# Kernel tuning notes

Hardware: AMD Instinct MI355X
Metric: run time of the kernel (lower is better)

The kernel has to match this reference:

```python
import jax, jax.numpy as jnp
import numpy as np

EMBED = 1024
HEADS = 16
HEAD_SIZE = 64


def setup_inputs() -> dict:
    key = jax.random.key(0)
    ks = jax.random.split(key, 6)
    B, T = 2, 2048
    s = EMBED ** -0.5
    x = jax.random.normal(ks[0], (B, T, EMBED), dtype=jnp.float32)
    Wk = jax.random.normal(ks[1], (EMBED, HEADS * HEAD_SIZE), dtype=jnp.float32) * s
    Wq = jax.random.normal(ks[2], (EMBED, HEADS * HEAD_SIZE), dtype=jnp.float32) * s
    Wv = jax.random.normal(ks[3], (EMBED, HEADS * HEAD_SIZE), dtype=jnp.float32) * s
    Wp = jax.random.normal(ks[4], (HEADS * HEAD_SIZE, EMBED), dtype=jnp.float32) * s
    bp = jax.random.normal(ks[5], (EMBED,), dtype=jnp.float32) * 0.01
    return {"x": x, "Wk": Wk, "Wq": Wq, "Wv": Wv, "Wp": Wp, "bp": bp}


def reference(x, Wk, Wq, Wv, Wp, bp):
    # x: [B, T, C]; dropout in eval mode (identity), matching inference semantics
    B, T, C = x.shape
    def split_heads(y):  # [B,T,H*Dh] -> [B,H,T,Dh]
        return y.reshape(B, T, HEADS, HEAD_SIZE).transpose(0, 2, 1, 3)
    q = split_heads(x @ Wq)
    k = split_heads(x @ Wk)
    v = split_heads(x @ Wv)
    scale = HEAD_SIZE ** -0.5
    wei = jnp.einsum('bhqd,bhkd->bhqk', q, k) * scale  # [B,H,T,T]
    causal = jnp.tril(jnp.ones((T, T), dtype=bool))
    wei = jnp.where(causal, wei, -jnp.inf)
    wei = jax.nn.softmax(wei, axis=-1)
    out = jnp.einsum('bhqk,bhkd->bhqd', wei, v)  # [B,H,T,Dh]
    out = out.transpose(0, 2, 1, 3).reshape(B, T, HEADS * HEAD_SIZE)
    return out @ Wp + bp
```

## Files before the change

kernel.cpp:

```cpp
#include <hip/hip_runtime.h>
#include <stdint.h>


typedef unsigned short bfu;
typedef unsigned int u32;
typedef short bf16x8 __attribute__((ext_vector_type(8)));
typedef float f32x4 __attribute__((ext_vector_type(4)));
typedef float f32x16 __attribute__((ext_vector_type(16)));

#define DEVI static __device__ __forceinline__

DEVI bfu f2bf(float f) {
  union { float f; unsigned u; } a; a.f = f;
  unsigned u = a.u;
  u += 0x7fffu + ((u >> 16) & 1u);
  return (bfu)(u >> 16);
}

DEVI float bf2f(bfu x) {
  union { u32 u; float f; } a; a.u = ((u32)x) << 16; return a.f;
}

DEVI void gld_lds16(const void* g, void* l) {
  __builtin_amdgcn_global_load_lds(
      (const __attribute__((address_space(1))) void*)g,
      (__attribute__((address_space(3))) void*)l, 16, 0, 0);
}

#define BAR_VM4()                                         \
  do {                                                    \
    asm volatile("s_waitcnt vmcnt(4)" ::: "memory");      \
    __builtin_amdgcn_s_barrier();                         \
    asm volatile("" ::: "memory");                        \
  } while (0)
#define BAR_VM0()                                         \
  do {                                                    \
    asm volatile("s_waitcnt vmcnt(0)" ::: "memory");      \
    __builtin_amdgcn_s_barrier();                         \
    asm volatile("" ::: "memory");                        \
  } while (0)


__global__ __launch_bounds__(256) void conv_x(const float* __restrict__ x,
                                              bfu* __restrict__ xb) {
  const int n4 = (4096 * 1024) / 4;
  for (int i = blockIdx.x * 256 + threadIdx.x; i < n4; i += gridDim.x * 256) {
    float4 v = ((const float4*)x)[i];
    ushort4 p;
    p.x = f2bf(v.x); p.y = f2bf(v.y); p.z = f2bf(v.z); p.w = f2bf(v.w);
    ((ushort4*)xb)[i] = p;
  }
}

__global__ __launch_bounds__(256) void conv_w(
    const float* __restrict__ W0, const float* __restrict__ W1,
    const float* __restrict__ W2, const float* __restrict__ W3,
    bfu* __restrict__ T0, bfu* __restrict__ T1,
    bfu* __restrict__ T2, bfu* __restrict__ T3) {
  __shared__ bfu tile[64][65];
  const float* W; bfu* T;
  switch (blockIdx.z) {
    case 0:  W = W0; T = T0; break;
    case 1:  W = W1; T = T1; break;
    case 2:  W = W2; T = T2; break;
    default: W = W3; T = T3; break;
  }
  const int k0 = blockIdx.y * 64, n0 = blockIdx.x * 64;
  const int c = threadIdx.x & 63, r4 = threadIdx.x >> 6;
#pragma unroll
  for (int i = 0; i < 16; i++) {
    int row = r4 + i * 4;
    tile[row][c] = f2bf(W[(size_t)(k0 + row) * 1024 + n0 + c]);
  }
  __syncthreads();
#pragma unroll
  for (int i = 0; i < 16; i++) {
    int row = r4 + i * 4;
    T[(size_t)(n0 + row) * 1024 + k0 + c] = tile[c][row];
  }
}


DEVI void gemm128_core(const bfu* __restrict__ A, const bfu* __restrict__ Bt,
                       int K, int m0, int n0, bfu* As, bfu* Bs, int tid,
                       f32x4 acc[4][4]) {
  const int lane = tid & 63, wave = tid >> 6;
  const int wr = wave >> 1, wc = wave & 1;
  const int fr = lane & 15, fq = lane >> 4;
  const int r_a = tid >> 2;
  const int koff = ((tid & 3) ^ ((tid >> 3) & 3)) * 8;
  const int rslot = (fq ^ ((fr >> 1) & 3)) * 8;
#define GSTAGE(buf, k0s)                                                              \
  do {                                                                                \
    gld_lds16(A  + (size_t)(m0 +      r_a) * K + (k0s) + koff,                        \
              As + (buf) * 4096 + tid * 8);                                           \
    gld_lds16(A  + (size_t)(m0 + 64 + r_a) * K + (k0s) + koff,                        \
              As + (buf) * 4096 + 2048 + tid * 8);                                    \
    gld_lds16(Bt + (size_t)(n0 +      r_a) * K + (k0s) + koff,                        \
              Bs + (buf) * 4096 + tid * 8);                                           \
    gld_lds16(Bt + (size_t)(n0 + 64 + r_a) * K + (k0s) + koff,                        \
              Bs + (buf) * 4096 + 2048 + tid * 8);                                    \
  } while (0)
  const int NS = K >> 5;
  GSTAGE(0, 0);
  GSTAGE(1, 32);
  BAR_VM4();
  for (int i = 0; i < NS; i++) {
    if (i + 2 < NS) GSTAGE((i + 2) % 3, (i + 2) * 32);
    const bfu* AsC = As + (i % 3) * 4096;
    const bfu* BsC = Bs + (i % 3) * 4096;
    bf16x8 af[4], bfv[4];
#pragma unroll
    for (int m = 0; m < 4; m++)
      af[m] = *(const bf16x8*)&AsC[(wr * 64 + m * 16 + fr) * 32 + rslot];
#pragma unroll
    for (int n = 0; n < 4; n++)
      bfv[n] = *(const bf16x8*)&BsC[(wc * 64 + n * 16 + fr) * 32 + rslot];
#pragma unroll
    for (int m = 0; m < 4; m++)
#pragma unroll
      for (int n = 0; n < 4; n++)
        acc[m][n] = __builtin_amdgcn_mfma_f32_16x16x32_bf16(af[m], bfv[n],
                                                            acc[m][n], 0, 0, 0);
    if (i + 2 < NS) BAR_VM4();
    else            BAR_VM0();
  }
#undef GSTAGE
}

__global__ __launch_bounds__(256) void gemm_qkv(
    const bfu* __restrict__ A, const bfu* __restrict__ Wqt,
    const bfu* __restrict__ Wkt, const bfu* __restrict__ Wvt,
    bfu* __restrict__ Qb, bfu* __restrict__ Kb, bfu* __restrict__ Vb) {
  __shared__ __align__(16) bfu As[3 * 4096];
  __shared__ __align__(16) bfu Bs[3 * 4096];
  const int bid = blockIdx.x;
  const int xcd = bid & 7, i0 = bid >> 3;
  const int tz = i0 >> 5, rem = i0 & 31;
  const int tx = rem >> 2, ty = xcd * 4 + (rem & 3);
  const bfu* Bt; bfu* out; int epi;
  if (tz == 0)      { Bt = Wqt; out = Qb; epi = 0; }
  else if (tz == 1) { Bt = Wkt; out = Kb; epi = 0; }
  else              { Bt = Wvt; out = Vb; epi = 1; }
  const float qs = (tz == 0) ? 0.1803368801f : 1.0f;
  const int m0 = ty * 128, n0 = tx * 128;
  const int tid = threadIdx.x, lane = tid & 63, wave = tid >> 6;
  const int wr = wave >> 1, wc = wave & 1, fr = lane & 15, fq = lane >> 4;
  f32x4 acc[4][4] = {};
  gemm128_core(A, Bt, 1024, m0, n0, As, Bs, tid, acc);
#pragma unroll
  for (int m = 0; m < 4; m++)
#pragma unroll
    for (int n = 0; n < 4; n++) {
      int r = m0 + wr * 64 + m * 16 + fq * 4;
      int c = n0 + wc * 64 + n * 16 + fr;
      int b = r >> 11, t = r & 2047, h = c >> 6, d = c & 63;
      if (epi == 0) {
        size_t base = ((size_t)(b * 16 + h) * 2048 + t) * 64 + d;
#pragma unroll
        for (int i = 0; i < 4; i++)
          out[base + (size_t)i * 64] = f2bf(acc[m][n][i] * qs);
      } else {
        size_t base = ((size_t)(b * 16 + h) * 64 + d) * 2048 + t;
        ushort4 p;
        p.x = f2bf(acc[m][n][0]); p.y = f2bf(acc[m][n][1]);
        p.z = f2bf(acc[m][n][2]); p.w = f2bf(acc[m][n][3]);
        *(ushort4*)&out[base] = p;
      }
    }
}

__global__ __launch_bounds__(256) void gemm_proj(
    const bfu* __restrict__ A, const bfu* __restrict__ Bt,
    const float* __restrict__ bias, float* __restrict__ out) {
  __shared__ __align__(16) bfu As[3 * 4096];
  __shared__ __align__(16) bfu Bs[3 * 4096];
  const int bid = blockIdx.x;
  const int xcd = bid & 7, i0 = bid >> 3;
  const int tx = i0 >> 2, ty = xcd * 4 + (i0 & 3);
  const int m0 = ty * 128, n0 = tx * 128;
  const int tid = threadIdx.x, lane = tid & 63, wave = tid >> 6;
  const int wr = wave >> 1, wc = wave & 1, fr = lane & 15, fq = lane >> 4;
  f32x4 acc[4][4] = {};
  gemm128_core(A, Bt, 1024, m0, n0, As, Bs, tid, acc);
#pragma unroll
  for (int m = 0; m < 4; m++)
#pragma unroll
    for (int n = 0; n < 4; n++) {
      int r = m0 + wr * 64 + m * 16 + fq * 4;
      int c = n0 + wc * 64 + n * 16 + fr;
      float bv = bias[c];
#pragma unroll
      for (int i = 0; i < 4; i++)
        out[(size_t)(r + i) * 1024 + c] = acc[m][n][i] + bv;
    }
}


__global__ __launch_bounds__(256) void attn_fwd(
    const bfu* __restrict__ Q, const bfu* __restrict__ K,
    const bfu* __restrict__ Vt, bfu* __restrict__ Ob,
    bfu* __restrict__ PO, float* __restrict__ PM, float* __restrict__ PL) {
  __shared__ __align__(16) bfu Ks[2][64 * 64];
  __shared__ __align__(16) bfu Vs[2][64 * 64];
  const int bid = blockIdx.x;
  const int xcd = bid & 7, i0 = bid >> 3;
  const int slot = i0 >> 5, cuL = i0 & 31;
  const int head = cuL >> 3, cu8 = cuL & 7;
  const int hb = xcd * 4 + head;
  int qb, mode;
  if (slot < 2)      { qb = 15 - cu8; mode = slot + 1; }
  else if (cu8 < 4)  { if (slot == 3) return; qb = cu8; mode = 0; }
  else               { qb = cu8; mode = slot - 1; }
  const int kb0   = (mode == 2) ? (qb + 1) : 0;
  const int kbmax = (mode == 1) ? qb : (2 * qb + 1);
  const int tid = threadIdx.x, wave = tid >> 6, lane = tid & 63;
  const int q31 = lane & 31, hi = lane >> 5;
  const bfu* Qh = Q  + (size_t)hb * 2048 * 64;
  const bfu* Kh = K  + (size_t)hb * 2048 * 64;
  const bfu* Vh = Vt + (size_t)hb * 64 * 2048;
  const int b = hb >> 4, h = hb & 15;
  const int q0w = qb * 128 + wave * 32;
  const int qg = q0w + q31;

  const int r0 = tid >> 3, r1 = (256 + tid) >> 3;
  const int c0 = (tid & 7) ^ (r0 & 7), c1 = (tid & 7) ^ (r1 & 7);
#define STAGE(bufi, kbase)                                                            \
  do {                                                                                \
    gld_lds16(Kh + (size_t)((kbase) + r0) * 64 + c0 * 8, &Ks[bufi][tid * 8]);         \
    gld_lds16(Kh + (size_t)((kbase) + r1) * 64 + c1 * 8, &Ks[bufi][(256 + tid) * 8]); \
    gld_lds16(Vh + (size_t)r0 * 2048 + (kbase) + c0 * 8, &Vs[bufi][tid * 8]);         \
    gld_lds16(Vh + (size_t)r1 * 2048 + (kbase) + c1 * 8, &Vs[bufi][(256 + tid) * 8]); \
  } while (0)

  bf16x8 qv[4];
#pragma unroll
  for (int c = 0; c < 4; c++)
    qv[c] = *(const bf16x8*)&Qh[(size_t)(q0w + q31) * 64 + c * 16 + hi * 8];

  bf16x8 onesv;
#pragma unroll
  for (int j = 0; j < 8; j++) onesv[j] = (short)0x3F80;

  f32x16 o0 = {}, o1 = {}, lac = {};
  float m = -1e30f;

  STAGE(0, kb0 * 64);
  __syncthreads();

  int cc = 0;
  for (int kb = kb0; kb <= kbmax; kb++, cc ^= 1) {
    const int cur = cc;
    if (kb < kbmax) STAGE(cur ^ 1, (kb + 1) * 64);
    const int kbase = kb * 64;
    if (kbase <= q0w + 31) {
      const bfu* KsC = Ks[cur];
      const bfu* VsC = Vs[cur];
      f32x16 s0 = {}, s1 = {};
#pragma unroll
      for (int c = 0; c < 4; c++) {
        const int g = 2 * c + hi;
        bf16x8 kf0 = *(const bf16x8*)&KsC[(q31 * 8 + (g ^ (q31 & 7))) * 8];
        bf16x8 kf1 = *(const bf16x8*)&KsC[((32 + q31) * 8 + (g ^ (q31 & 7))) * 8];
        s0 = __builtin_amdgcn_mfma_f32_32x32x16_bf16(kf0, qv[c], s0, 0, 0, 0);
        s1 = __builtin_amdgcn_mfma_f32_32x32x16_bf16(kf1, qv[c], s1, 0, 0, 0);
      }
      if (kbase + 63 > q0w) {
#pragma unroll
        for (int r = 0; r < 16; r++) {
          int krow = (r & 3) + 8 * (r >> 2) + 4 * hi;
          if (kbase + krow > qg)      s0[r] = -1e30f;
          if (kbase + 32 + krow > qg) s1[r] = -1e30f;
        }
      }
      float pm = s0[0];
#pragma unroll
      for (int r = 1; r < 16; r++) pm = fmaxf(pm, s0[r]);
#pragma unroll
      for (int r = 0; r < 16; r++) pm = fmaxf(pm, s1[r]);
      pm = fmaxf(pm, __shfl_xor(pm, 32));
      if (!__all(pm <= m + 8.0f)) {
        float mn = fmaxf(m, pm);
        float al = __builtin_amdgcn_exp2f(m - mn);
        m = mn;
#pragma unroll
        for (int r = 0; r < 16; r++) {
          float alq = __shfl(al, (r & 3) + 8 * (r >> 2) + 4 * hi);
          o0[r] *= alq; o1[r] *= alq; lac[r] *= alq;
        }
      }
      u32 W0[8], W1[8];
#pragma unroll
      for (int w = 0; w < 8; w++) {
        float a0 = __builtin_amdgcn_exp2f(s0[2 * w] - m);
        float a1 = __builtin_amdgcn_exp2f(s0[2 * w + 1] - m);
        asm("v_cvt_pk_bf16_f32 %0, %1, %2" : "=v"(W0[w]) : "v"(a0), "v"(a1));
        float b0 = __builtin_amdgcn_exp2f(s1[2 * w] - m);
        float b1 = __builtin_amdgcn_exp2f(s1[2 * w + 1] - m);
        asm("v_cvt_pk_bf16_f32 %0, %1, %2" : "=v"(W1[w]) : "v"(b0), "v"(b1));
      }
      __builtin_amdgcn_s_setprio(1);
#pragma unroll
      for (int c = 0; c < 4; c++) {
        const u32* Wsel = (c < 2) ? W0 : W1;
        const int w0 = 4 * (c & 1);
        u32 t0 = Wsel[w0],     t2 = Wsel[w0 + 2];
        u32 t1 = Wsel[w0 + 1], t3 = Wsel[w0 + 3];
        asm("v_permlane32_swap_b32 %0, %1" : "+v"(t0), "+v"(t2));
        asm("v_permlane32_swap_b32 %0, %1" : "+v"(t1), "+v"(t3));
        union { u32 u[4]; bf16x8 v; } pa;
        pa.u[0] = t0; pa.u[1] = t1; pa.u[2] = t2; pa.u[3] = t3;
        const int g = 2 * c + hi;
        bf16x8 vb0 = *(const bf16x8*)&VsC[(q31 * 8 + (g ^ (q31 & 7))) * 8];
        bf16x8 vb1 = *(const bf16x8*)&VsC[((32 + q31) * 8 + (g ^ (q31 & 7))) * 8];
        o0  = __builtin_amdgcn_mfma_f32_32x32x16_bf16(pa.v, vb0,   o0,  0, 0, 0);
        o1  = __builtin_amdgcn_mfma_f32_32x32x16_bf16(pa.v, vb1,   o1,  0, 0, 0);
        lac = __builtin_amdgcn_mfma_f32_32x32x16_bf16(pa.v, onesv, lac, 0, 0, 0);
      }
      __builtin_amdgcn_s_setprio(0);
    }
    __syncthreads();
  }
#undef STAGE

  if (mode == 0) {
#pragma unroll
    for (int r = 0; r < 16; r++) {
      int t = q0w + (r & 3) + 8 * (r >> 2) + 4 * hi;
      float inv = 1.0f / lac[r];
      size_t base = (size_t)(b * 2048 + t) * 1024 + h * 64;
      Ob[base + q31]      = f2bf(o0[r] * inv);
      Ob[base + 32 + q31] = f2bf(o1[r] * inv);
    }
  } else {
    const int p = (hb * 12 + (qb - 4)) * 2 + (mode - 1);
    bfu*   po = PO + (size_t)p * 8192;
    float* pmv = PM + p * 128;
    float* plv = PL + p * 128;
    pmv[wave * 32 + q31] = m;
#pragma unroll
    for (int r = 0; r < 16; r++) {
      int rm = (r & 3) + 8 * (r >> 2) + 4 * hi;
      plv[wave * 32 + rm] = lac[r];
      po[(wave * 32 + rm) * 64 + q31]      = f2bf(o0[r]);
      po[(wave * 32 + rm) * 64 + 32 + q31] = f2bf(o1[r]);
    }
  }
}

__global__ __launch_bounds__(256) void attn_comb(
    const bfu* __restrict__ PO, const float* __restrict__ PM,
    const float* __restrict__ PL, bfu* __restrict__ Ob) {
  const int g = blockIdx.x;
  const int hb = g / 12, j = g % 12, qb = j + 4;
  const int b = hb >> 4, h = hb & 15;
  const int p0 = g * 2, p1 = p0 + 1;
  const int tid = threadIdx.x;
  const int r = tid >> 1, ch = tid & 1;
  float m0 = PM[p0 * 128 + r], m1 = PM[p1 * 128 + r];
  float l0 = PL[p0 * 128 + r], l1 = PL[p1 * 128 + r];
  float ms = fmaxf(m0, m1);
  float f0 = __builtin_amdgcn_exp2f(m0 - ms);
  float f1 = __builtin_amdgcn_exp2f(m1 - ms);
  float inv = 1.0f / (l0 * f0 + l1 * f1);
  const bfu* a0 = PO + (size_t)p0 * 8192 + r * 64 + ch * 32;
  const bfu* a1 = PO + (size_t)p1 * 8192 + r * 64 + ch * 32;
  const int t = qb * 128 + r;
  bfu* ob = Ob + (size_t)(b * 2048 + t) * 1024 + h * 64 + ch * 32;
#pragma unroll
  for (int k = 0; k < 4; k++) {
    bf16x8 v0 = *(const bf16x8*)(a0 + k * 8);
    bf16x8 v1 = *(const bf16x8*)(a1 + k * 8);
    bf16x8 vo;
#pragma unroll
    for (int e = 0; e < 8; e++) {
      float acc = bf2f((bfu)(unsigned short)v0[e]) * f0 +
                  bf2f((bfu)(unsigned short)v1[e]) * f1;
      vo[e] = (short)f2bf(acc * inv);
    }
    *(bf16x8*)(ob + k * 8) = vo;
  }
}


extern "C" void kernel_launch(void* const* d_in, const int* in_sizes, int n_in,
                              void* d_out, int out_size, void* d_ws, size_t ws_size,
                              hipStream_t stream) {
  const float* x  = (const float*)d_in[0];
  const float* Wk = (const float*)d_in[1];
  const float* Wq = (const float*)d_in[2];
  const float* Wv = (const float*)d_in[3];
  const float* Wp = (const float*)d_in[4];
  const float* bp = (const float*)d_in[5];
  char* ws = (char*)d_ws;
  bfu* xb  = (bfu*)(ws);
  bfu* Wqt = (bfu*)(ws + ( 8u << 20));
  bfu* Wkt = (bfu*)(ws + (10u << 20));
  bfu* Wvt = (bfu*)(ws + (12u << 20));
  bfu* Wpt = (bfu*)(ws + (14u << 20));
  bfu* Qb  = (bfu*)(ws + (16u << 20));
  bfu* Kb  = (bfu*)(ws + (24u << 20));
  bfu* Vb  = (bfu*)(ws + (32u << 20));
  bfu* Ab  = (bfu*)(ws + (40u << 20));
  bfu*   PO = (bfu*)(ws);
  float* PM = (float*)(ws + (13u << 20));
  float* PL = (float*)(ws + (13u << 20) + (512u << 10));
  float* out = (float*)d_out;

  conv_x<<<1024, 256, 0, stream>>>(x, xb);
  conv_w<<<dim3(16, 16, 4), 256, 0, stream>>>(Wq, Wk, Wv, Wp, Wqt, Wkt, Wvt, Wpt);
  gemm_qkv<<<768, 256, 0, stream>>>(xb, Wqt, Wkt, Wvt, Qb, Kb, Vb);
  attn_fwd<<<1024, 256, 0, stream>>>(Qb, Kb, Vb, Ab, PO, PM, PL);
  attn_comb<<<384, 256, 0, stream>>>(PO, PM, PL, Ab);
  gemm_proj<<<256, 256, 0, stream>>>(Ab, Wpt, bp, out);
}
```

Before: 136.1 us.

## Replace QKV GEMM with a fused 256x256-tile double-buffered 512-thread kernel

Replaces the 128x128-tile QKV projection with one kernel that treats the contiguous transposed Wq/Wk/Wv as a single 3072-wide B matrix. It computes 256x256 output tiles with 8 waves and double-buffered LDS staging. Global-to-LDS loads for the next K tile are interleaved with MFMA quarters, and s_setprio raises priority during the MFMA bursts. The aim is more operand reuse per load and better overlap of loads with compute. The risk is that only 192 workgroups are launched, fewer than the CU count, which leaves some CUs idle, and the larger accumulator footprint puts pressure on registers.

```diff
diff --git a/kernel.cpp b/kernel.cpp
--- a/kernel.cpp
+++ b/kernel.cpp
@@ -78,6 +78,120 @@
     int row = r4 + i * 4;
     T[(size_t)(n0 + row) * 1024 + k0 + c] = tile[c][row];
   }
+}
+
+
+__global__ __launch_bounds__(512) void gemm_qkv256(
+    const bfu* __restrict__ A, const bfu* __restrict__ Bt,
+    bfu* __restrict__ Qb, bfu* __restrict__ Kb, bfu* __restrict__ Vb) {
+  __shared__ __align__(16) bfu LDS[2 * 32768];
+  const int bid = blockIdx.x;
+  const int xcd = bid & 7, i0 = bid >> 3;
+  const int tx = i0 >> 1, ty = xcd * 2 + (i0 & 1);
+  const int z = tx >> 2;
+  const int m0 = ty * 256, n0g = tx * 256;
+  const int tid = threadIdx.x, wave = tid >> 6, lane = tid & 63;
+  const int wr = wave >> 2, wc = wave & 3;
+  const int fr = lane & 15, fq = lane >> 4;
+  const int rslot4 = fq ^ ((fr >> 1) & 3);
+
+#define STAGE_HT(bufn, ktile, isB, kk)                                           \
+  do {                                                                           \
+    const bfu* srcb = (isB) ? Bt + (size_t)n0g * 1024 : A + (size_t)m0 * 1024;   \
+    bfu* dstb = LDS + (bufn) * 32768 + ((isB) ? 16384 : 0) + (kk) * 8192;        \
+    _Pragma("unroll")                                                            \
+    for (int j_ = 0; j_ < 2; j_++) {                                             \
+      int s_ = tid + j_ * 512;                                                   \
+      int r_ = s_ >> 2, cg_ = (s_ & 3) ^ ((r_ >> 1) & 3);                        \
+      gld_lds16(srcb + (size_t)r_ * 1024 + (ktile) * 64 + (kk) * 32 + cg_ * 8,   \
+                dstb + s_ * 8);                                                  \
+    }                                                                            \
+  } while (0)
+
+#define READ_B(kk)                                                               \
+  _Pragma("unroll")                                                              \
+  for (int n = 0; n < 4; n++)                                                    \
+    bfv[n] = *(const bf16x8*)&bufc_p[16384 + (kk) * 8192 +                       \
+              ((wc * 64 + n * 16 + fr) * 4 + rslot4) * 8];
+
+#define READ_A(dst, mq, kk)                                                      \
+  _Pragma("unroll")                                                              \
+  for (int mm = 0; mm < 4; mm++)                                                 \
+    dst[mm] = *(const bf16x8*)&bufc_p[(kk) * 8192 +                              \
+              ((wr * 128 + ((mq) * 4 + mm) * 16 + fr) * 4 + rslot4) * 8];
+
+#define MFMA_Q(afv, mq)                                                          \
+  __builtin_amdgcn_s_setprio(1);                                                 \
+  _Pragma("unroll")                                                              \
+  for (int mm = 0; mm < 4; mm++)                                                 \
+    _Pragma("unroll")                                                            \
+    for (int n = 0; n < 4; n++)                                                  \
+      acc[(mq) * 4 + mm][n] = __builtin_amdgcn_mfma_f32_16x16x32_bf16(           \
+          afv[mm], bfv[n], acc[(mq) * 4 + mm][n], 0, 0, 0);                      \
+  __builtin_amdgcn_s_setprio(0);
+
+  f32x4 acc[8][4] = {};
+  STAGE_HT(0, 0, 0, 0);
+  STAGE_HT(0, 0, 1, 0);
+  STAGE_HT(0, 0, 0, 1);
+  STAGE_HT(0, 0, 1, 1);
+  BAR_VM4();
+
+  const int NT = 16;
+  for (int t = 0; t < NT; t++) {
+    const int more = (t + 1 < NT);
+    const bfu* bufc_p = LDS + (t & 1) * 32768;
+    const int bufn = (t & 1) ^ 1;
+    bf16x8 bfv[4], afA[4], afB[4];
+    READ_B(0);
+    READ_A(afA, 0, 0);
+    if (more) STAGE_HT(bufn, t + 1, 0, 0);
+    MFMA_Q(afA, 0);
+    READ_A(afB, 1, 0);
+    if (more) STAGE_HT(bufn, t + 1, 1, 0);
+    MFMA_Q(afB, 1);
+    if (more) BAR_VM4();
+    else      BAR_VM0();
+    READ_B(1);
+    READ_A(afA, 0, 1);
+    if (more) STAGE_HT(bufn, t + 1, 0, 1);
+    MFMA_Q(afA, 0);
+    READ_A(afB, 1, 1);
+    if (more) STAGE_HT(bufn, t + 1, 1, 1);
+    MFMA_Q(afB, 1);
+    BAR_VM4();
+  }
+#undef STAGE_HT
+#undef READ_B
+#undef READ_A
+#undef MFMA_Q
+
+  const float qs = (z == 0) ? 0.1803368801f : 1.0f;
+#pragma unroll
+  for (int mf = 0; mf < 8; mf++)
+#pragma unroll
+    for (int n = 0; n < 4; n++) {
+      int r = m0 + wr * 128 + mf * 16 + fq * 4;
+      int cwm = (tx & 3) * 256 + wc * 64 + n * 16 + fr;
+      int b = r >> 11, tt = r & 2047, h = cwm >> 6, d = cwm & 63;
+      if (z == 0) {
+        size_t base = ((size_t)(b * 16 + h) * 2048 + tt) * 64 + d;
+#pragma unroll
+        for (int i = 0; i < 4; i++)
+          Qb[base + (size_t)i * 64] = f2bf(acc[mf][n][i] * qs);
+      } else if (z == 1) {
+        size_t base = ((size_t)(b * 16 + h) * 2048 + tt) * 64 + d;
+#pragma unroll
+        for (int i = 0; i < 4; i++)
+          Kb[base + (size_t)i * 64] = f2bf(acc[mf][n][i]);
+      } else {
+        size_t base = ((size_t)(b * 16 + h) * 64 + d) * 2048 + tt;
+        ushort4 p;
+        p.x = f2bf(acc[mf][n][0]); p.y = f2bf(acc[mf][n][1]);
+        p.z = f2bf(acc[mf][n][2]); p.w = f2bf(acc[mf][n][3]);
+        *(ushort4*)&Vb[base] = p;
+      }
+    }
 }
 
 
@@ -128,48 +242,6 @@
 #undef GSTAGE
 }
 
-__global__ __launch_bounds__(256) void gemm_qkv(
-    const bfu* __restrict__ A, const bfu* __restrict__ Wqt,
-    const bfu* __restrict__ Wkt, const bfu* __restrict__ Wvt,
-    bfu* __restrict__ Qb, bfu* __restrict__ Kb, bfu* __restrict__ Vb) {
-  __shared__ __align__(16) bfu As[3 * 4096];
-  __shared__ __align__(16) bfu Bs[3 * 4096];
-  const int bid = blockIdx.x;
-  const int xcd = bid & 7, i0 = bid >> 3;
-  const int tz = i0 >> 5, rem = i0 & 31;
-  const int tx = rem >> 2, ty = xcd * 4 + (rem & 3);
-  const bfu* Bt; bfu* out; int epi;
-  if (tz == 0)      { Bt = Wqt; out = Qb; epi = 0; }
-  else if (tz == 1) { Bt = Wkt; out = Kb; epi = 0; }
-  else              { Bt = Wvt; out = Vb; epi = 1; }
-  const float qs = (tz == 0) ? 0.1803368801f : 1.0f;
-  const int m0 = ty * 128, n0 = tx * 128;
-  const int tid = threadIdx.x, lane = tid & 63, wave = tid >> 6;
-  const int wr = wave >> 1, wc = wave & 1, fr = lane & 15, fq = lane >> 4;
-  f32x4 acc[4][4] = {};
-  gemm128_core(A, Bt, 1024, m0, n0, As, Bs, tid, acc);
-#pragma unroll
-  for (int m = 0; m < 4; m++)
-#pragma unroll
-    for (int n = 0; n < 4; n++) {
-      int r = m0 + wr * 64 + m * 16 + fq * 4;
-      int c = n0 + wc * 64 + n * 16 + fr;
-      int b = r >> 11, t = r & 2047, h = c >> 6, d = c & 63;
-      if (epi == 0) {
-        size_t base = ((size_t)(b * 16 + h) * 2048 + t) * 64 + d;
-#pragma unroll
-        for (int i = 0; i < 4; i++)
-          out[base + (size_t)i * 64] = f2bf(acc[m][n][i] * qs);
-      } else {
-        size_t base = ((size_t)(b * 16 + h) * 64 + d) * 2048 + t;
-        ushort4 p;
-        p.x = f2bf(acc[m][n][0]); p.y = f2bf(acc[m][n][1]);
-        p.z = f2bf(acc[m][n][2]); p.w = f2bf(acc[m][n][3]);
-        *(ushort4*)&out[base] = p;
-      }
-    }
-}
-
 __global__ __launch_bounds__(256) void gemm_proj(
     const bfu* __restrict__ A, const bfu* __restrict__ Bt,
     const float* __restrict__ bias, float* __restrict__ out) {
@@ -409,7 +481,7 @@
 
   conv_x<<<1024, 256, 0, stream>>>(x, xb);
   conv_w<<<dim3(16, 16, 4), 256, 0, stream>>>(Wq, Wk, Wv, Wp, Wqt, Wkt, Wvt, Wpt);
-  gemm_qkv<<<768, 256, 0, stream>>>(xb, Wqt, Wkt, Wvt, Qb, Kb, Vb);
+  gemm_qkv256<<<192, 512, 0, stream>>>(xb, Wqt, Qb, Kb, Vb);
   attn_fwd<<<1024, 256, 0, stream>>>(Qb, Kb, Vb, Ab, PO, PM, PL);
   attn_comb<<<384, 256, 0, stream>>>(PO, PM, PL, Ab);
   gemm_proj<<<256, 256, 0, stream>>>(Ab, Wpt, bp, out);
```

Measured after the change: 121.7 us. 1.12x faster.
